# Performance work log

Measured on AMD Instinct MI355X. Metric: run time of the kernel, lower is better.

The kernel has to match this reference:

```python
import jax, jax.numpy as jnp
import numpy as np

E = 500_000   # num edges
X = 128       # x_ind (node feat dim)
EA = 64       # edge_ind
U = 64        # u_ind
HS = 256      # hidden size
B = 64        # num graphs
CIN = 2 * X + EA + U  # 384
EPS = 1e-5


def setup_inputs() -> dict:
    key = jax.random.key(0)
    ks = jax.random.split(key, 12)
    src = jax.random.normal(ks[0], (E, X), jnp.float32)
    dst = jax.random.normal(ks[1], (E, X), jnp.float32)
    edge_attr = jax.random.normal(ks[2], (E, EA), jnp.float32)
    u = jax.random.normal(ks[3], (B, U), jnp.float32)
    batch = jnp.sort(jax.random.randint(ks[4], (E,), 0, B))
    # Conv1d(k=1) == per-edge linear; weights [Cin, Cout]
    W1 = jax.random.normal(ks[5], (CIN, HS), jnp.float32) / np.sqrt(CIN)
    b1 = jnp.zeros((HS,), jnp.float32)
    g1 = jnp.ones((HS,), jnp.float32)   # BatchNorm1d gamma
    be1 = jnp.zeros((HS,), jnp.float32)  # BatchNorm1d beta
    W2 = jax.random.normal(ks[6], (HS, HS), jnp.float32) / np.sqrt(HS)
    b2 = jnp.zeros((HS,), jnp.float32)
    g2 = jnp.ones((HS,), jnp.float32)
    be2 = jnp.zeros((HS,), jnp.float32)
    return dict(src=src, dst=dst, edge_attr=edge_attr, u=u,
                W1=W1, b1=b1, g1=g1, be1=be1,
                W2=W2, b2=b2, g2=g2, be2=be2, batch=batch)


def _batchnorm(x, gamma, beta):
    # training-mode BN over the edge (batch) axis, biased variance, per-channel
    mean = jnp.mean(x, axis=0)
    var = jnp.mean(jnp.square(x - mean), axis=0)
    return (x - mean) * (gamma / jnp.sqrt(var + EPS)) + beta


def reference(src, dst, edge_attr, u, W1, b1, g1, be1, W2, b2, g2, be2, batch):
    feats = jnp.concatenate([src, dst, edge_attr, u[batch]], axis=-1)
    h = feats @ W1 + b1                 # Conv1d k=1 layer 1
    h = jax.nn.relu(_batchnorm(h, g1, be1))
    # dropout is identity in eval / deterministic reference
    out = h @ W2 + b2                   # Conv1d k=1 layer 2
    out = _batchnorm(out, g2, be2)
    return out                          # [E, HS]
```

## Files before the change

### kernel.cpp

```cpp
#include <hip/hip_runtime.h>
#include <stdint.h>

#define E_EDGES 500000
#define NB 7813
#define EPS_BN 1e-5f
#define FXS  268435456.0f
#define FXSI (1.0 / 268435456.0)

typedef __attribute__((ext_vector_type(8))) _Float16 h8_t;
typedef __attribute__((ext_vector_type(4))) float  f4_t;
typedef __attribute__((ext_vector_type(8))) unsigned short us8;
typedef __attribute__((ext_vector_type(4))) unsigned short us4;
typedef __attribute__((ext_vector_type(4))) float  fl4;
typedef unsigned short u16;
typedef unsigned int   u32;
typedef unsigned long long u64;

__device__ __forceinline__ float bf2f(u16 x) { return __uint_as_float(((u32)x) << 16); }
__device__ __forceinline__ u16 f2h(float f) {
    _Float16 h = (_Float16)f;
    return __builtin_bit_cast(u16, h);
}
__device__ __forceinline__ float h2f(u16 x) {
    _Float16 h = __builtin_bit_cast(_Float16, x);
    return (float)h;
}

__device__ __forceinline__ int dtype_of(const u32* g1w) {
    u32 w = g1w[0];
    return (w == 0x3F800000u) ? 0 : (w == 0x3F803F80u) ? 1 : (w == 0x3C003C00u) ? 2 : 0;
}

struct A4 { fl4 f0, f1, f2, f3; };

__global__ void prep_k(const u32* __restrict__ g1probe,
                       const void* __restrict__ W1, const void* __restrict__ W2,
                       const void* __restrict__ b1, const void* __restrict__ g1,
                       const void* __restrict__ be1, const void* __restrict__ b2,
                       const void* __restrict__ g2, const void* __restrict__ be2,
                       u16* __restrict__ W1T, u16* __restrict__ W2T,
                       float* __restrict__ smallF, u64* __restrict__ isums) {
    const int d = dtype_of(g1probe);
    int i = blockIdx.x * 256 + threadIdx.x;
    if (i < 256 * 384) {
        int n = i / 384, k = i % 384;
        float v = (d == 1) ? bf2f(((const u16*)W1)[k * 256 + n])
                : (d == 2) ? h2f(((const u16*)W1)[k * 256 + n])
                           : ((const float*)W1)[k * 256 + n];
        W1T[i] = f2h(v);
        return;
    }
    int j = i - 256 * 384;
    if (j < 256 * 256) {
        int n = j / 256, k = j % 256;
        float v = (d == 1) ? bf2f(((const u16*)W2)[k * 256 + n])
                : (d == 2) ? h2f(((const u16*)W2)[k * 256 + n])
                           : ((const float*)W2)[k * 256 + n];
        W2T[j] = f2h(v);
        return;
    }
    int k = j - 256 * 256;
    if (k < 1536) {
        int vec = k >> 8, c = k & 255;
        const void* s = vec == 0 ? b1 : vec == 1 ? g1 : vec == 2 ? be1
                      : vec == 3 ? b2 : vec == 4 ? g2 : be2;
        smallF[k] = (d == 1) ? bf2f(((const u16*)s)[c])
                  : (d == 2) ? h2f(((const u16*)s)[c])
                             : ((const float*)s)[c];
        return;
    }
    int z = k - 1536;
    if (z < 1024) isums[z] = 0ull;
}

__global__ __launch_bounds__(256, 3) void gemm1_k(
    const void* __restrict__ srcp, const void* __restrict__ dstp,
    const void* __restrict__ eap,  const void* __restrict__ up,
    const u32* __restrict__ g1probe, const int* __restrict__ batch,
    const u16* __restrict__ W1T, const float* __restrict__ b1F,
    u16* __restrict__ h_out, u64* __restrict__ isums)
{
    __shared__ u16 As[64 * 64];
    __shared__ u16 Bs[256 * 64];
    const int t  = threadIdx.x;
    const int w  = t >> 6;
    const int l  = t & 63;
    const int lr = l & 15;
    const int lg = l >> 4;
    const int row0 = blockIdx.x * 64;
    const int d = dtype_of(g1probe);

    const int rl = t >> 2;
    const int cq = (t & 3) * 16;
    int grow = row0 + rl;
    grow = grow < E_EDGES ? grow : (E_EDGES - 1);
    const int gb = batch[grow];

    auto loadA = [&](int s) -> A4 {
        size_t eo; const void* base;
        if (s < 2)      { eo = (size_t)grow * 128 + s * 64 + cq;       base = srcp; }
        else if (s < 4) { eo = (size_t)grow * 128 + (s - 2) * 64 + cq; base = dstp; }
        else if (s == 4){ eo = (size_t)grow * 64 + cq;                 base = eap; }
        else            { eo = (size_t)gb * 64 + cq;                   base = up; }
        A4 a;
        if (d == 0) {
            const float* p = (const float*)base + eo;
            a.f0 = *(const fl4*)p;       a.f1 = *(const fl4*)(p + 4);
            a.f2 = *(const fl4*)(p + 8); a.f3 = *(const fl4*)(p + 12);
        } else {
            const u16* p = (const u16*)base + eo;
            a.f0 = __builtin_bit_cast(fl4, *(const us8*)p);
            a.f1 = __builtin_bit_cast(fl4, *(const us8*)(p + 8));
        }
        return a;
    };
    auto storeA = [&](A4 a) {
        us8 o0, o1;
        if (d == 0) {
#pragma unroll
            for (int j = 0; j < 4; ++j) {
                o0[j] = f2h(a.f0[j]); o0[j + 4] = f2h(a.f1[j]);
                o1[j] = f2h(a.f2[j]); o1[j + 4] = f2h(a.f3[j]);
            }
        } else if (d == 1) {
            us8 r0 = __builtin_bit_cast(us8, a.f0);
            us8 r1 = __builtin_bit_cast(us8, a.f1);
#pragma unroll
            for (int j = 0; j < 8; ++j) { o0[j] = f2h(bf2f(r0[j])); o1[j] = f2h(bf2f(r1[j])); }
        } else {
            o0 = __builtin_bit_cast(us8, a.f0);
            o1 = __builtin_bit_cast(us8, a.f1);
        }
        const int sw = (rl & 7) << 3;
        *(us8*)&As[rl * 64 + (cq ^ sw)]       = o0;
        *(us8*)&As[rl * 64 + ((cq + 8) ^ sw)] = o1;
    };

    f4_t acc[4][4];
#pragma unroll
    for (int m = 0; m < 4; ++m)
#pragma unroll
        for (int n = 0; n < 4; ++n) { acc[m][n][0]=0.f; acc[m][n][1]=0.f; acc[m][n][2]=0.f; acc[m][n][3]=0.f; }

    A4 ca = loadA(0);
#pragma unroll
    for (int s = 0; s < 6; ++s) {
        storeA(ca);
#pragma unroll
        for (int i = 0; i < 8; ++i) {
            int cid = i * 256 + t;
            int n = cid >> 3, c8 = (cid & 7) * 8;
            us8 v = *(const us8*)(W1T + (size_t)n * 384 + s * 64 + c8);
            *(us8*)&Bs[n * 64 + (c8 ^ ((n & 7) << 3))] = v;
        }
        __syncthreads();
        A4 na;
        if (s < 5) na = loadA(s + 1);
#pragma unroll
        for (int kk = 0; kk < 64; kk += 32) {
            const int kc = (kk + lg * 8) ^ ((lr & 7) << 3);
            h8_t a[4], b[4];
#pragma unroll
            for (int m = 0; m < 4; ++m) a[m] = *(const h8_t*)&As[(m * 16 + lr) * 64 + kc];
#pragma unroll
            for (int n = 0; n < 4; ++n) b[n] = *(const h8_t*)&Bs[(w * 64 + n * 16 + lr) * 64 + kc];
#pragma unroll
            for (int m = 0; m < 4; ++m)
#pragma unroll
                for (int n = 0; n < 4; ++n)
                    acc[m][n] = __builtin_amdgcn_mfma_f32_16x16x32_f16(a[m], b[n], acc[m][n], 0, 0, 0);
        }
        __syncthreads();
        ca = na;
    }

    float b1f[4];
#pragma unroll
    for (int n = 0; n < 4; ++n) b1f[n] = b1F[w * 64 + n * 16 + lr];

    float S[4], Q[4];
#pragma unroll
    for (int n = 0; n < 4; ++n) { S[n] = 0.f; Q[n] = 0.f; }
#pragma unroll
    for (int m = 0; m < 4; ++m) {
#pragma unroll
        for (int j = 0; j < 4; ++j) {
            int r = row0 + m * 16 + lg * 4 + j;
            bool valid = r < E_EDGES;
#pragma unroll
            for (int n = 0; n < 4; ++n) {
                float v = acc[m][n][j] + b1f[n];
                if (valid) {
                    h_out[(size_t)r * 512 + (w * 64 + n * 16 + lr)] = f2h(v);
                    S[n] += v; Q[n] += v * v;
                }
            }
        }
    }
#pragma unroll
    for (int n = 0; n < 4; ++n) {
        S[n] += __shfl_xor(S[n], 16); S[n] += __shfl_xor(S[n], 32);
        Q[n] += __shfl_xor(Q[n], 16); Q[n] += __shfl_xor(Q[n], 32);
    }
    if (l < 16) {
#pragma unroll
        for (int n = 0; n < 4; ++n) {
            int col = w * 64 + n * 16 + l;
            atomicAdd(&isums[col],       (u64)(long long)llrintf(S[n] * FXS));
            atomicAdd(&isums[256 + col], (u64)(long long)llrintf(Q[n] * FXS));
        }
    }
}

__global__ void bnstats_k(const u64* __restrict__ isums,
                          const float* __restrict__ gF, const float* __restrict__ beF,
                          float* __restrict__ sc, float* __restrict__ sh)
{
    int c = threadIdx.x;
    double S = (double)(long long)isums[c]       * FXSI;
    double Q = (double)(long long)isums[256 + c] * FXSI;
    double mean = S / (double)E_EDGES;
    double var  = Q / (double)E_EDGES - mean * mean;
    float inv  = rsqrtf((float)var + EPS_BN);
    float scale = gF[c] * inv;
    sc[c] = scale;
    sh[c] = beF[c] - (float)mean * scale;
}

__global__ __launch_bounds__(256, 3) void gemm2_k(
    u16* h_io, const u16* __restrict__ W2T,
    const float* __restrict__ sc1, const float* __restrict__ sh1,
    const float* __restrict__ b2F, u64* __restrict__ isums)
{
    __shared__ u16 As[64 * 64];
    __shared__ u16 Bs[256 * 64];
    __shared__ float scs[256], shs[256];
    const int t  = threadIdx.x;
    const int w  = t >> 6;
    const int l  = t & 63;
    const int lr = l & 15;
    const int lg = l >> 4;
    const int row0 = blockIdx.x * 64;

    const int rl = t >> 2;
    const int cq = (t & 3) * 16;
    int grow = row0 + rl;
    grow = grow < E_EDGES ? grow : (E_EDGES - 1);

    f4_t acc[4][4];
#pragma unroll
    for (int m = 0; m < 4; ++m)
#pragma unroll
        for (int n = 0; n < 4; ++n) { acc[m][n][0]=0.f; acc[m][n][1]=0.f; acc[m][n][2]=0.f; acc[m][n][3]=0.f; }

    scs[t] = sc1[t]; shs[t] = sh1[t];
    us8 ca0 = *(const us8*)(h_io + (size_t)grow * 512 + cq);
    us8 ca1 = *(const us8*)(h_io + (size_t)grow * 512 + cq + 8);
    __syncthreads();

#pragma unroll
    for (int s = 0; s < 4; ++s) {
        {
            const int sw = (rl & 7) << 3;
            int k0 = s * 64 + cq;
            fl4 s0 = *(const fl4*)&scs[k0],     s1 = *(const fl4*)&scs[k0 + 4];
            fl4 s2 = *(const fl4*)&scs[k0 + 8], s3 = *(const fl4*)&scs[k0 + 12];
            fl4 h0 = *(const fl4*)&shs[k0],     h1 = *(const fl4*)&shs[k0 + 4];
            fl4 h2 = *(const fl4*)&shs[k0 + 8], h3 = *(const fl4*)&shs[k0 + 12];
            us8 o0, o1;
#pragma unroll
            for (int j = 0; j < 4; ++j) {
                o0[j]     = f2h(fmaxf(h2f(ca0[j])     * s0[j] + h0[j], 0.f));
                o0[j + 4] = f2h(fmaxf(h2f(ca0[j + 4]) * s1[j] + h1[j], 0.f));
                o1[j]     = f2h(fmaxf(h2f(ca1[j])     * s2[j] + h2[j], 0.f));
                o1[j + 4] = f2h(fmaxf(h2f(ca1[j + 4]) * s3[j] + h3[j], 0.f));
            }
            *(us8*)&As[rl * 64 + (cq ^ sw)]       = o0;
            *(us8*)&As[rl * 64 + ((cq + 8) ^ sw)] = o1;
        }
#pragma unroll
        for (int i = 0; i < 8; ++i) {
            int cid = i * 256 + t;
            int n = cid >> 3, c8 = (cid & 7) * 8;
            us8 v = *(const us8*)(W2T + (size_t)n * 256 + s * 64 + c8);
            *(us8*)&Bs[n * 64 + (c8 ^ ((n & 7) << 3))] = v;
        }
        __syncthreads();
        us8 na0, na1;
        if (s < 3) {
            na0 = *(const us8*)(h_io + (size_t)grow * 512 + (s + 1) * 64 + cq);
            na1 = *(const us8*)(h_io + (size_t)grow * 512 + (s + 1) * 64 + cq + 8);
        }
#pragma unroll
        for (int kk = 0; kk < 64; kk += 32) {
            const int kc = (kk + lg * 8) ^ ((lr & 7) << 3);
            h8_t a[4], b[4];
#pragma unroll
            for (int m = 0; m < 4; ++m) a[m] = *(const h8_t*)&As[(m * 16 + lr) * 64 + kc];
#pragma unroll
            for (int n = 0; n < 4; ++n) b[n] = *(const h8_t*)&Bs[(w * 64 + n * 16 + lr) * 64 + kc];
#pragma unroll
            for (int m = 0; m < 4; ++m)
#pragma unroll
                for (int n = 0; n < 4; ++n)
                    acc[m][n] = __builtin_amdgcn_mfma_f32_16x16x32_f16(a[m], b[n], acc[m][n], 0, 0, 0);
        }
        __syncthreads();
        ca0 = na0; ca1 = na1;
    }

    float b2f[4];
#pragma unroll
    for (int n = 0; n < 4; ++n) b2f[n] = b2F[w * 64 + n * 16 + lr];

    float S[4], Q[4];
#pragma unroll
    for (int n = 0; n < 4; ++n) { S[n] = 0.f; Q[n] = 0.f; }
#pragma unroll
    for (int m = 0; m < 4; ++m) {
#pragma unroll
        for (int j = 0; j < 4; ++j) {
            int r = row0 + m * 16 + lg * 4 + j;
            bool valid = r < E_EDGES;
#pragma unroll
            for (int n = 0; n < 4; ++n) {
                float v = acc[m][n][j] + b2f[n];
                if (valid) {
                    h_io[(size_t)r * 512 + (w * 64 + n * 16 + lr)] = f2h(v);
                    S[n] += v; Q[n] += v * v;
                }
            }
        }
    }
#pragma unroll
    for (int n = 0; n < 4; ++n) {
        S[n] += __shfl_xor(S[n], 16); S[n] += __shfl_xor(S[n], 32);
        Q[n] += __shfl_xor(Q[n], 16); Q[n] += __shfl_xor(Q[n], 32);
    }
    if (l < 16) {
#pragma unroll
        for (int n = 0; n < 4; ++n) {
            int col = w * 64 + n * 16 + l;
            atomicAdd(&isums[col],       (u64)(long long)llrintf(S[n] * FXS));
            atomicAdd(&isums[256 + col], (u64)(long long)llrintf(Q[n] * FXS));
        }
    }
}

__global__ __launch_bounds__(256) void bnapply_k(u16* outH, float* outF,
        const float* __restrict__ sc, const float* __restrict__ sh)
{
    const int lane = threadIdx.x & 63;
    const int c0 = lane * 4;
    long long wave = (long long)blockIdx.x * 4 + (threadIdx.x >> 6);
    long long nwaves = (long long)gridDim.x * 4;
    fl4 s = *(const fl4*)&sc[c0];
    fl4 h = *(const fl4*)&sh[c0];
    for (long long r = wave; r < E_EDGES; r += nwaves) {
        us4 x = *(const us4*)(outH + r * 512 + c0);
        fl4 y;
#pragma unroll
        for (int j = 0; j < 4; ++j) y[j] = h2f(x[j]) * s[j] + h[j];
        *(fl4*)(outF + r * 256 + c0) = y;
    }
}

extern "C" void kernel_launch(void* const* d_in, const int* in_sizes, int n_in,
                              void* d_out, int out_size, void* d_ws, size_t ws_size,
                              hipStream_t stream)
{
    const void* srcp = d_in[0];
    const void* dstp = d_in[1];
    const void* eap  = d_in[2];
    const void* up   = d_in[3];
    const void* W1   = d_in[4];
    const void* b1   = d_in[5];
    const void* g1   = d_in[6];
    const void* be1  = d_in[7];
    const void* W2   = d_in[8];
    const void* b2   = d_in[9];
    const void* g2   = d_in[10];
    const void* be2  = d_in[11];
    const int* batch = (const int*)d_in[12];
    float* outF = (float*)d_out;
    u16*   outH = (u16*)d_out;

    char* ws = (char*)d_ws;
    size_t off = 0;
    u16* W1T = (u16*)(ws + off); off += (size_t)256 * 384 * 2;
    u16* W2T = (u16*)(ws + off); off += (size_t)256 * 256 * 2;
    u64* isums = (u64*)(ws + off); off += 1024 * 8;
    float* smallF = (float*)(ws + off); off += 1536 * 4;
    float* sc1 = (float*)(ws + off); off += 1024;
    float* sh1 = (float*)(ws + off); off += 1024;
    float* sc2 = (float*)(ws + off); off += 1024;
    float* sh2 = (float*)(ws + off); off += 1024;

    const float* b1F  = smallF;
    const float* g1F  = smallF + 256;
    const float* be1F = smallF + 512;
    const float* b2F  = smallF + 768;
    const float* g2F  = smallF + 1024;
    const float* be2F = smallF + 1280;

    prep_k<<<651, 256, 0, stream>>>((const u32*)g1, W1, W2, b1, g1, be1, b2, g2, be2,
                                    W1T, W2T, smallF, isums);
    gemm1_k<<<NB, 256, 0, stream>>>(srcp, dstp, eap, up, (const u32*)g1, batch,
                                    W1T, b1F, outH, isums);
    bnstats_k<<<1, 256, 0, stream>>>(isums, g1F, be1F, sc1, sh1);
    gemm2_k<<<NB, 256, 0, stream>>>(outH, W2T, sc1, sh1, b2F, isums + 512);
    bnstats_k<<<1, 256, 0, stream>>>(isums + 512, g2F, be2F, sc2, sh2);
    bnapply_k<<<2048, 256, 0, stream>>>(outH, outF, sc2, sh2);
}
```

Baseline: 639.0 us.

## Load GEMM weight fragments directly from global into registers, drop LDS B tile

Both GEMM kernels stop staging the full 256x64 weight tile in shared memory each K-step. Each wave now loads its own MFMA B fragments straight from global memory (W1T/W2T, which should stay L2-resident) into registers. This removes the LDS writes and reads for B and cuts shared memory from about 40KB to 8KB per block, which may allow higher occupancy. In exchange there are more uncoalesced global loads of small weight rows per wave, and their latency sits just before the MFMAs with little prefetching to hide it.

```diff
diff --git a/kernel.cpp b/kernel.cpp
--- a/kernel.cpp
+++ b/kernel.cpp
@@ -81,7 +81,6 @@
     u16* __restrict__ h_out, u64* __restrict__ isums)
 {
     __shared__ u16 As[64 * 64];
-    __shared__ u16 Bs[256 * 64];
     const int t  = threadIdx.x;
     const int w  = t >> 6;
     const int l  = t & 63;
@@ -95,6 +94,8 @@
     int grow = row0 + rl;
     grow = grow < E_EDGES ? grow : (E_EDGES - 1);
     const int gb = batch[grow];
+
+    const u16* wbase = W1T + (size_t)(w * 64 + lr) * 384 + lg * 8;
 
     auto loadA = [&](int s) -> A4 {
         size_t eo; const void* base;
@@ -146,29 +147,33 @@
 #pragma unroll
     for (int s = 0; s < 6; ++s) {
         storeA(ca);
-#pragma unroll
-        for (int i = 0; i < 8; ++i) {
-            int cid = i * 256 + t;
-            int n = cid >> 3, c8 = (cid & 7) * 8;
-            us8 v = *(const us8*)(W1T + (size_t)n * 384 + s * 64 + c8);
-            *(us8*)&Bs[n * 64 + (c8 ^ ((n & 7) << 3))] = v;
-        }
         __syncthreads();
         A4 na;
         if (s < 5) na = loadA(s + 1);
+        const u16* wp = wbase + s * 64;
+        h8_t bA0 = *(const h8_t*)(wp);
+        h8_t bA1 = *(const h8_t*)(wp + 16 * 384);
+        h8_t bA2 = *(const h8_t*)(wp + 32 * 384);
+        h8_t bA3 = *(const h8_t*)(wp + 48 * 384);
+        h8_t bB0 = *(const h8_t*)(wp + 32);
+        h8_t bB1 = *(const h8_t*)(wp + 16 * 384 + 32);
+        h8_t bB2 = *(const h8_t*)(wp + 32 * 384 + 32);
+        h8_t bB3 = *(const h8_t*)(wp + 48 * 384 + 32);
 #pragma unroll
         for (int kk = 0; kk < 64; kk += 32) {
             const int kc = (kk + lg * 8) ^ ((lr & 7) << 3);
-            h8_t a[4], b[4];
+            h8_t a[4];
 #pragma unroll
             for (int m = 0; m < 4; ++m) a[m] = *(const h8_t*)&As[(m * 16 + lr) * 64 + kc];
-#pragma unroll
-            for (int n = 0; n < 4; ++n) b[n] = *(const h8_t*)&Bs[(w * 64 + n * 16 + lr) * 64 + kc];
-#pragma unroll
-            for (int m = 0; m < 4; ++m)
-#pragma unroll
-                for (int n = 0; n < 4; ++n)
-                    acc[m][n] = __builtin_amdgcn_mfma_f32_16x16x32_f16(a[m], b[n], acc[m][n], 0, 0, 0);
+            h8_t b0 = kk ? bB0 : bA0, b1 = kk ? bB1 : bA1;
+            h8_t b2 = kk ? bB2 : bA2, b3 = kk ? bB3 : bA3;
+#pragma unroll
+            for (int m = 0; m < 4; ++m) {
+                acc[m][0] = __builtin_amdgcn_mfma_f32_16x16x32_f16(a[m], b0, acc[m][0], 0, 0, 0);
+                acc[m][1] = __builtin_amdgcn_mfma_f32_16x16x32_f16(a[m], b1, acc[m][1], 0, 0, 0);
+                acc[m][2] = __builtin_amdgcn_mfma_f32_16x16x32_f16(a[m], b2, acc[m][2], 0, 0, 0);
+                acc[m][3] = __builtin_amdgcn_mfma_f32_16x16x32_f16(a[m], b3, acc[m][3], 0, 0, 0);
+            }
         }
         __syncthreads();
         ca = na;
@@ -233,7 +238,6 @@
     const float* __restrict__ b2F, u64* __restrict__ isums)
 {
     __shared__ u16 As[64 * 64];
-    __shared__ u16 Bs[256 * 64];
     __shared__ float scs[256], shs[256];
     const int t  = threadIdx.x;
     const int w  = t >> 6;
@@ -246,6 +250,8 @@
     const int cq = (t & 3) * 16;
     int grow = row0 + rl;
     grow = grow < E_EDGES ? grow : (E_EDGES - 1);
+
+    const u16* wbase = W2T + (size_t)(w * 64 + lr) * 256 + lg * 8;
 
     f4_t acc[4][4];
 #pragma unroll
@@ -278,32 +284,36 @@
             *(us8*)&As[rl * 64 + (cq ^ sw)]       = o0;
             *(us8*)&As[rl * 64 + ((cq + 8) ^ sw)] = o1;
         }
-#pragma unroll
-        for (int i = 0; i < 8; ++i) {
-            int cid = i * 256 + t;
-            int n = cid >> 3, c8 = (cid & 7) * 8;
-            us8 v = *(const us8*)(W2T + (size_t)n * 256 + s * 64 + c8);
-            *(us8*)&Bs[n * 64 + (c8 ^ ((n & 7) << 3))] = v;
-        }
         __syncthreads();
         us8 na0, na1;
         if (s < 3) {
             na0 = *(const us8*)(h_io + (size_t)grow * 512 + (s + 1) * 64 + cq);
             na1 = *(const us8*)(h_io + (size_t)grow * 512 + (s + 1) * 64 + cq + 8);
         }
+        const u16* wp = wbase + s * 64;
+        h8_t bA0 = *(const h8_t*)(wp);
+        h8_t bA1 = *(const h8_t*)(wp + 16 * 256);
+        h8_t bA2 = *(const h8_t*)(wp + 32 * 256);
+        h8_t bA3 = *(const h8_t*)(wp + 48 * 256);
+        h8_t bB0 = *(const h8_t*)(wp + 32);
+        h8_t bB1 = *(const h8_t*)(wp + 16 * 256 + 32);
+        h8_t bB2 = *(const h8_t*)(wp + 32 * 256 + 32);
+        h8_t bB3 = *(const h8_t*)(wp + 48 * 256 + 32);
 #pragma unroll
         for (int kk = 0; kk < 64; kk += 32) {
             const int kc = (kk + lg * 8) ^ ((lr & 7) << 3);
-            h8_t a[4], b[4];
+            h8_t a[4];
 #pragma unroll
             for (int m = 0; m < 4; ++m) a[m] = *(const h8_t*)&As[(m * 16 + lr) * 64 + kc];
-#pragma unroll
-            for (int n = 0; n < 4; ++n) b[n] = *(const h8_t*)&Bs[(w * 64 + n * 16 + lr) * 64 + kc];
-#pragma unroll
-            for (int m = 0; m < 4; ++m)
-#pragma unroll
-                for (int n = 0; n < 4; ++n)
-                    acc[m][n] = __builtin_amdgcn_mfma_f32_16x16x32_f16(a[m], b[n], acc[m][n], 0, 0, 0);
+            h8_t b0 = kk ? bB0 : bA0, b1 = kk ? bB1 : bA1;
+            h8_t b2 = kk ? bB2 : bA2, b3 = kk ? bB3 : bA3;
+#pragma unroll
+            for (int m = 0; m < 4; ++m) {
+                acc[m][0] = __builtin_amdgcn_mfma_f32_16x16x32_f16(a[m], b0, acc[m][0], 0, 0, 0);
+                acc[m][1] = __builtin_amdgcn_mfma_f32_16x16x32_f16(a[m], b1, acc[m][1], 0, 0, 0);
+                acc[m][2] = __builtin_amdgcn_mfma_f32_16x16x32_f16(a[m], b2, acc[m][2], 0, 0, 0);
+                acc[m][3] = __builtin_amdgcn_mfma_f32_16x16x32_f16(a[m], b3, acc[m][3], 0, 0, 0);
+            }
         }
         __syncthreads();
         ca0 = na0; ca1 = na1;
```

Measured after the change: 766.5 us. 19.9% more time.
